# Kernel optimization log

Measured on AMD Instinct MI355X. Metric: run time of the kernel, lower is better.

The kernel has to match this reference:

```python
import jax, jax.numpy as jnp
import numpy as np

B, N, S = 256, 512, 32
D_ENT, D_KEY, D_IN, D_FUNC, D_TYPE, H = 256, 32, 1024, 256, 259, 32


def _init_linear(k, out_d, in_d):
    kw, kb = jax.random.split(k)
    bound = 1.0 / np.sqrt(in_d)
    W = jax.random.uniform(kw, (out_d, in_d), minval=-bound, maxval=bound, dtype=jnp.float32)
    b = jax.random.uniform(kb, (out_d,), minval=-bound, maxval=bound, dtype=jnp.float32)
    return W, b


def setup_inputs() -> dict:
    key = jax.random.key(0)
    ks = jax.random.split(key, 16)
    inp = {
        "embedding": jax.random.normal(ks[0], (B, D_IN), jnp.float32),
        "available_unit_type_mask": (jax.random.uniform(ks[1], (B, D_TYPE)) < 0.5).astype(jnp.float32),
        "available_units_mask": jnp.ones((B, N), jnp.float32),
        "entity_embedding": jax.random.normal(ks[2], (B, N, D_ENT), jnp.float32),
        "selected_units": jax.random.randint(ks[3], (B, S), 0, N, dtype=jnp.int32),
        "end_embedding": jax.random.uniform(ks[4], (1, D_KEY), minval=-1.0, maxval=1.0, dtype=jnp.float32) / np.sqrt(D_KEY),
    }
    inp["W_key"], inp["b_key"] = _init_linear(ks[5], D_KEY, D_ENT)
    inp["W_func"], inp["b_func"] = _init_linear(ks[6], D_FUNC, D_TYPE)
    inp["W_fc1"], inp["b_fc1"] = _init_linear(ks[7], D_FUNC, D_IN)
    inp["W_fc2"], inp["b_fc2"] = _init_linear(ks[8], D_KEY, D_FUNC)
    inp["W_embed"], inp["b_embed"] = _init_linear(ks[9], D_IN, D_KEY)
    inp["W_ih"], inp["b_ih"] = _init_linear(ks[10], 4 * H, D_KEY)
    inp["W_hh"], inp["b_hh"] = _init_linear(ks[11], 4 * H, H)
    return inp


def reference(embedding, available_unit_type_mask, available_units_mask, entity_embedding,
              selected_units, end_embedding, W_key, b_key, W_func, b_func, W_fc1, b_fc1,
              W_fc2, b_fc2, W_embed, b_embed, W_ih, b_ih, W_hh, b_hh):
    Bv, Nv, _ = entity_embedding.shape
    Sv = selected_units.shape[1]
    # keys for each entity + end-flag embedding appended -> [B, N+1, key_dim]
    key_t = jnp.einsum('bnd,kd->bnk', entity_embedding, W_key) + b_key
    end = jnp.broadcast_to(end_embedding[None, :, :], (Bv, 1, end_embedding.shape[1]))
    pad_key = jnp.concatenate([key_t, end], axis=1)
    # mask: entities + end flag; teacher-forced selected positions forced to 1
    mask0 = jnp.concatenate([available_units_mask, jnp.ones((Bv, 1), available_units_mask.dtype)], axis=1)
    mask0 = mask0.at[jnp.arange(Bv)[:, None], selected_units].set(1.0)
    func_embed = jax.nn.relu(available_unit_type_mask @ W_func.T + b_func)
    inv_n = 1.0 / jnp.float32(Nv)  # split_entity_num = end_flag_index = num_units
    bidx = jnp.arange(Bv)
    # per-step selected index (dummy 0 on the final end-flag step) and validity
    sel_seq = jnp.concatenate([selected_units.T, jnp.zeros((1, Bv), selected_units.dtype)], axis=0)
    valid_seq = jnp.concatenate([jnp.ones((Sv, Bv), jnp.float32), jnp.zeros((1, Bv), jnp.float32)], axis=0)

    def step(carry, xs):
        emb, h, c, mask = carry
        sel, valid = xs
        # query = fc2(relu(fc1(emb) + func_embed))
        x = jax.nn.relu(emb @ W_fc1.T + b_fc1 + func_embed) @ W_fc2.T + b_fc2
        # one LSTM step
        gates = x @ W_ih.T + b_ih + h @ W_hh.T + b_hh
        i_g, f_g, g_g, o_g = jnp.split(gates, 4, axis=1)
        c = jax.nn.sigmoid(f_g) * c + jax.nn.sigmoid(i_g) * jnp.tanh(g_g)
        h = jax.nn.sigmoid(o_g) * jnp.tanh(c)
        # masked dot-product over keys -> logits [B, N+1]
        q = jnp.einsum('bk,bnk->bn', h, pad_key) - (1.0 - mask) * 1e9
        # mark selected unit unavailable for subsequent steps
        mask = mask.at[bidx, sel].set(jnp.where(valid > 0, 0.0, mask[bidx, sel]))
        # one-hot gather of selected key, averaged, fed back into embedding
        emb_sel = pad_key[bidx, sel] * inv_n
        emb = emb + (emb_sel @ W_embed.T + b_embed) * valid[:, None]
        return (emb, h, c, mask), q

    h0 = jnp.zeros((Bv, W_hh.shape[1]), jnp.float32)
    c0 = jnp.zeros_like(h0)
    (emb, _, _, _), logits = jax.lax.scan(step, (embedding, h0, c0, mask0), (sel_seq, valid_seq))
    logits = jnp.transpose(logits, (1, 0, 2))  # [B, S+1, N+1]
    return logits, emb
```

## Files before the change

kernel.cpp:

```cpp
#include <hip/hip_runtime.h>
#include <math.h>

#define BB_ 256
#define NN_ 512
#define SS_ 32
#define NP1 513
#define SP1 33
#define D_IN 1024
#define D_TYPE 259
#define INV_N (1.0f/512.0f)

typedef short s16x4 __attribute__((ext_vector_type(4)));
typedef short s16x8 __attribute__((ext_vector_type(8)));
typedef float f32x4 __attribute__((ext_vector_type(4)));

#if defined(__has_builtin)
#if __has_builtin(__builtin_amdgcn_rcpf)
#define FRCP(x) __builtin_amdgcn_rcpf(x)
#else
#define FRCP(x) (1.0f / (x))
#endif
#else
#define FRCP(x) (1.0f / (x))
#endif

__device__ __forceinline__ float fsig(float x) { return FRCP(1.0f + __expf(-x)); }
__device__ __forceinline__ float ftanh(float x) { return fmaf(-2.0f, FRCP(1.0f + __expf(2.0f * x)), 1.0f); }
__device__ __forceinline__ short f2bf(float f) {
    unsigned u = __float_as_uint(f);
    unsigned r = (u + 0x7FFFu + ((u >> 16) & 1u)) >> 16;
    return (short)r;
}

__global__ __launch_bounds__(256) void prep_kernel(
    const float* __restrict__ Wemb, const float* __restrict__ bemb,
    const float* __restrict__ Wfc1, const float* __restrict__ emb0,
    const float* __restrict__ bfc1, const float* __restrict__ atm,
    const float* __restrict__ Wf, const float* __restrict__ bf,
    float* __restrict__ WcombT, float* __restrict__ cbv,
    float* __restrict__ act_pre)
{
    __shared__ float col[D_IN];
    __shared__ float a_lds[16 * 260];
    __shared__ float w_lds[16 * 260];
    const int tid = threadIdx.x;

    if (blockIdx.x < 33) {
        const int k = blockIdx.x;
        if (k < 32) {
            for (int p = 0; p < 4; p++) col[p * 256 + tid] = Wemb[(size_t)(p * 256 + tid) * 32 + k];
        } else {
            for (int p = 0; p < 4; p++) col[p * 256 + tid] = bemb[p * 256 + tid];
        }
        __syncthreads();
        const float* wr = Wfc1 + (size_t)tid * D_IN;
        float acc = 0.0f;
        for (int i4 = 0; i4 < 256; i4++) {
            float4 wv = *(const float4*)(wr + i4 * 4);
            acc = fmaf(col[i4*4+0], wv.x, acc);
            acc = fmaf(col[i4*4+1], wv.y, acc);
            acc = fmaf(col[i4*4+2], wv.z, acc);
            acc = fmaf(col[i4*4+3], wv.w, acc);
        }
        if (k < 32) WcombT[tid * 32 + k] = acc;
        else        cbv[tid] = acc;
    } else {
        const int idx = blockIdx.x - 33;
        const int jt = idx & 15, bt = idx >> 4;
        const int bb = tid >> 4, jj = tid & 15;

#pragma unroll 4
        for (int r = 0; r < 16; r++) {
            a_lds[r * 260 + tid] = atm[(size_t)(bt * 16 + r) * D_TYPE + tid];
            w_lds[r * 260 + tid] = Wf[(size_t)(jt * 16 + r) * D_TYPE + tid];
            if (tid < 3) {
                a_lds[r * 260 + 256 + tid] = atm[(size_t)(bt * 16 + r) * D_TYPE + 256 + tid];
                w_lds[r * 260 + 256 + tid] = Wf[(size_t)(jt * 16 + r) * D_TYPE + 256 + tid];
            }
        }
        __syncthreads();
        float accf = 0.0f;
        {
            const float4* ap = (const float4*)&a_lds[bb * 260];
            const float4* wp = (const float4*)&w_lds[jj * 260];
#pragma unroll 8
            for (int i4 = 0; i4 < 64; i4++) {
                float4 a = ap[i4]; float4 wv = wp[i4];
                accf = fmaf(a.x, wv.x, accf); accf = fmaf(a.y, wv.y, accf);
                accf = fmaf(a.z, wv.z, accf); accf = fmaf(a.w, wv.w, accf);
            }
            for (int i = 256; i < 259; i++) accf = fmaf(a_lds[bb * 260 + i], w_lds[jj * 260 + i], accf);
        }
        float acc = 0.0f;
        for (int c = 0; c < 4; c++) {
            __syncthreads();
#pragma unroll
            for (int p = 0; p < 4; p++) {
                int l4 = p * 256 + tid;
                int r = l4 >> 6, k4 = l4 & 63;
                *(float4*)&a_lds[r * 260 + k4 * 4] =
                    *(const float4*)(emb0 + (size_t)(bt * 16 + r) * D_IN + c * 256 + k4 * 4);
                *(float4*)&w_lds[r * 260 + k4 * 4] =
                    *(const float4*)(Wfc1 + (size_t)(jt * 16 + r) * D_IN + c * 256 + k4 * 4);
            }
            __syncthreads();
#pragma unroll 8
            for (int k4 = 0; k4 < 64; k4++) {
                float4 a = *(const float4*)&a_lds[bb * 260 + k4 * 4];
                float4 wv = *(const float4*)&w_lds[jj * 260 + k4 * 4];
                acc = fmaf(a.x, wv.x, acc); acc = fmaf(a.y, wv.y, acc);
                acc = fmaf(a.z, wv.z, acc); acc = fmaf(a.w, wv.w, acc);
            }
        }
        const int b = bt * 16 + bb, j = jt * 16 + jj;
        act_pre[b * 256 + j] = acc + bfc1[j] + fmaxf(accf + bf[j], 0.0f);
    }
}

__global__ __launch_bounds__(256, 1) void mega_kernel(
    const float* __restrict__ ent, const float* __restrict__ Wk,
    const float* __restrict__ bk, const float* __restrict__ endv,
    const float* __restrict__ act_pre0, const int* __restrict__ sel,
    const float* __restrict__ Wfc2, const float* __restrict__ bfc2,
    const float* __restrict__ Wih, const float* __restrict__ bih,
    const float* __restrict__ bhh, const float* __restrict__ Whh,
    const float* __restrict__ WcombT, const float* __restrict__ cbv,
    const float* __restrict__ emb0, const float* __restrict__ Wemb,
    const float* __restrict__ bemb, const float* __restrict__ avail,
    float* __restrict__ logits, float* __restrict__ emb_out)
{
    __shared__ float k_l[NP1 * 33];
    __shared__ float u_l[17028];
    __shared__ float x_l[SP1 * 32];
    __shared__ float h_all[SP1 * 32];
    __shared__ float cumE_l[SP1 * 32];
    __shared__ float m0_l[NP1];
    __shared__ int   tf_l[NP1];
    __shared__ float ssel_l[32];

    short* a_st  = (short*)u_l;
    float* rap_l = u_l;
    float* red_l = u_l + 8580;
    float* xg_l  = u_l;

    const int tid = threadIdx.x;
    const int b = blockIdx.x;
    const int lane = tid & 63, w = tid >> 6;
    const int nl = lane & 15, q = lane >> 4;

    {
        s16x8 bfr[8][2];
#pragma unroll
        for (int s = 0; s < 8; s++)
#pragma unroll
            for (int t = 0; t < 2; t++) {
                const float* src = Wk + (size_t)(t * 16 + nl) * 256 + s * 32 + q * 8;
                float4 v0 = *(const float4*)(src);
                float4 v1 = *(const float4*)(src + 4);
                s16x8 bv;
                bv[0] = f2bf(v0.x); bv[1] = f2bf(v0.y); bv[2] = f2bf(v0.z); bv[3] = f2bf(v0.w);
                bv[4] = f2bf(v1.x); bv[5] = f2bf(v1.y); bv[6] = f2bf(v1.z); bv[7] = f2bf(v1.w);
                bfr[s][t] = bv;
            }
        float bkv[2];
        bkv[0] = bk[nl]; bkv[1] = bk[16 + nl];
        const float* entb = ent + (size_t)b * NN_ * 256;

        for (int chunk = 0; chunk < 4; ++chunk) {
            f32x4 acc[2][2];
#pragma unroll
            for (int mt = 0; mt < 2; mt++)
#pragma unroll
                for (int t = 0; t < 2; t++) acc[mt][t] = (f32x4)0.0f;

            for (int kc = 0; kc < 4; ++kc) {
                __syncthreads();
#pragma unroll
                for (int p = 0; p < 8; p++) {
                    int flat = p * 256 + tid;
                    int row = flat >> 4;
                    int f4 = flat & 15;
                    float4 v = *(const float4*)(entb + (size_t)(chunk * 128 + row) * 256 + kc * 64 + f4 * 4);
                    s16x4 sv;
                    sv[0] = f2bf(v.x); sv[1] = f2bf(v.y); sv[2] = f2bf(v.z); sv[3] = f2bf(v.w);
                    *(s16x4*)&a_st[row * 72 + f4 * 4] = sv;
                }
                __syncthreads();
#pragma unroll
                for (int ks = 0; ks < 2; ks++) {
                    const int sg = kc * 2 + ks;
#pragma unroll
                    for (int mt = 0; mt < 2; mt++) {
                        s16x8 af = *(const s16x8*)&a_st[(w * 32 + mt * 16 + nl) * 72 + ks * 32 + q * 8];
#pragma unroll
                        for (int t = 0; t < 2; t++)
                            acc[mt][t] = __builtin_amdgcn_mfma_f32_16x16x32_bf16(af, bfr[sg][t], acc[mt][t], 0, 0, 0);
                    }
                }
            }
#pragma unroll
            for (int mt = 0; mt < 2; mt++)
#pragma unroll
                for (int t = 0; t < 2; t++)
#pragma unroll
                    for (int r = 0; r < 4; r++) {
                        int n = chunk * 128 + w * 32 + mt * 16 + q * 4 + r;
                        k_l[n * 33 + t * 16 + nl] = acc[mt][t][r] + bkv[t];
                    }
        }
        if (tid < 32) k_l[512 * 33 + tid] = endv[tid];
        for (int n = tid; n < NP1; n += 256) {
            m0_l[n] = (n < NN_) ? avail[(size_t)b * NN_ + n] : 1.0f;
            tf_l[n] = 1000;
        }
    }
    __syncthreads();

    {
        const int k = tid & 31, sq = tid >> 5;
        const int sq4 = sq * 4;
        float v0, v1, v2, v3;
        {
            int s0 = sel[b * SS_ + sq4 + 0];
            int s1 = sel[b * SS_ + sq4 + 1];
            int s2 = sel[b * SS_ + sq4 + 2];
            int s3 = sel[b * SS_ + sq4 + 3];
            v0 = k_l[s0 * 33 + k] * INV_N;
            v1 = k_l[s1 * 33 + k] * INV_N;
            v2 = k_l[s2 * 33 + k] * INV_N;
            v3 = k_l[s3 * 33 + k] * INV_N;
        }
        float p0 = v0, p1 = p0 + v1, p2 = p1 + v2, p3 = p2 + v3;
        x_l[sq * 32 + k] = p3;
        if (tid < SS_) {
            int n = sel[b * SS_ + tid];
            m0_l[n] = 1.0f;
            atomicMin(&tf_l[n], tid);
        }
        __syncthreads();
        float off = 0.0f;
        for (int p = 0; p < 8; p++) if (p < sq) off += x_l[p * 32 + k];
        cumE_l[(sq4 + 1) * 32 + k] = off + p0;
        cumE_l[(sq4 + 2) * 32 + k] = off + p1;
        cumE_l[(sq4 + 3) * 32 + k] = off + p2;
        cumE_l[(sq4 + 4) * 32 + k] = off + p3;
        if (tid < 32) cumE_l[tid] = 0.0f;
        if (sq == 7) ssel_l[k] = off + p3;
    }
    __syncthreads();

    {
        float wcr[32];
#pragma unroll
        for (int k4 = 0; k4 < 8; k4++) {
            float4 v = *(const float4*)(WcombT + (size_t)tid * 32 + k4 * 4);
            wcr[k4*4] = v.x; wcr[k4*4+1] = v.y; wcr[k4*4+2] = v.z; wcr[k4*4+3] = v.w;
        }
        const float cbr = cbv[tid];
        const float ap0v = act_pre0[b * 256 + tid];
        for (int t = 0; t < SP1; ++t) {
            float ap = fmaf((float)t, cbr, ap0v);
            const float4* ce = (const float4*)&cumE_l[t * 32];
#pragma unroll
            for (int k4 = 0; k4 < 8; k4++) {
                float4 e = ce[k4];
                ap = fmaf(e.x, wcr[k4*4], ap);   ap = fmaf(e.y, wcr[k4*4+1], ap);
                ap = fmaf(e.z, wcr[k4*4+2], ap); ap = fmaf(e.w, wcr[k4*4+3], ap);
            }
            rap_l[t * 260 + tid] = fmaxf(ap, 0.0f);
        }
    }
    __syncthreads();

    {
        const int seg = tid >> 5, i = tid & 31;
        float wfc2r[32];
#pragma unroll
        for (int i4 = 0; i4 < 8; i4++) {
            float4 v = *(const float4*)(Wfc2 + (size_t)i * 256 + seg * 32 + i4 * 4);
            wfc2r[i4*4] = v.x; wfc2r[i4*4+1] = v.y; wfc2r[i4*4+2] = v.z; wfc2r[i4*4+3] = v.w;
        }
        for (int t = 0; t < SP1; ++t) {
            float part = 0.0f;
            const float4* rp = (const float4*)&rap_l[t * 260 + seg * 32];
#pragma unroll
            for (int i4 = 0; i4 < 8; i4++) {
                float4 rv = rp[i4];
                part = fmaf(rv.x, wfc2r[i4*4], part);   part = fmaf(rv.y, wfc2r[i4*4+1], part);
                part = fmaf(rv.z, wfc2r[i4*4+2], part); part = fmaf(rv.w, wfc2r[i4*4+3], part);
            }
            red_l[t * 256 + seg * 32 + i] = part;
        }
    }
    __syncthreads();

    for (int p = 0; p < 5; p++) {
        int idx = p * 256 + tid;
        if (idx < SP1 * 32) {
            int t = idx >> 5, i = idx & 31;
            float x = bfc2[i];
#pragma unroll
            for (int s = 0; s < 8; s++) x += red_l[t * 256 + s * 32 + i];
            x_l[t * 32 + i] = x;
        }
    }
    __syncthreads();

    {
        const int g = tid & 127, half = tid >> 7;
        float wihr[32];
#pragma unroll
        for (int k4 = 0; k4 < 8; k4++) {
            float4 v = *(const float4*)(Wih + (size_t)g * 32 + k4 * 4);
            wihr[k4*4] = v.x; wihr[k4*4+1] = v.y; wihr[k4*4+2] = v.z; wihr[k4*4+3] = v.w;
        }
        const float bihg = bih[g] + bhh[g];
        for (int t = half; t < SP1; t += 2) {
            float gg = bihg;
            const float4* xp = (const float4*)&x_l[t * 32];
#pragma unroll
            for (int k4 = 0; k4 < 8; k4++) {
                float4 xv = xp[k4];
                gg = fmaf(xv.x, wihr[k4*4], gg);   gg = fmaf(xv.y, wihr[k4*4+1], gg);
                gg = fmaf(xv.z, wihr[k4*4+2], gg); gg = fmaf(xv.w, wihr[k4*4+3], gg);
            }
            xg_l[t * 128 + g] = gg;
        }
    }
    __syncthreads();

    if (tid < 64) {
        float whh0[32], whh1[32];
#pragma unroll
        for (int k4 = 0; k4 < 8; k4++) {
            float4 v0 = *(const float4*)(Whh + (size_t)tid * 32 + k4 * 4);
            float4 v1 = *(const float4*)(Whh + (size_t)(tid + 64) * 32 + k4 * 4);
            whh0[k4*4] = v0.x; whh0[k4*4+1] = v0.y; whh0[k4*4+2] = v0.z; whh0[k4*4+3] = v0.w;
            whh1[k4*4] = v1.x; whh1[k4*4+1] = v1.y; whh1[k4*4+2] = v1.z; whh1[k4*4+3] = v1.w;
        }
        float c = 0.0f, h = 0.0f;
        for (int t = 0; t < SP1; ++t) {
            float g0 = xg_l[t * 128 + tid];
            float g1 = xg_l[t * 128 + 64 + tid];
            if (t > 0) {
#pragma unroll
                for (int k = 0; k < 32; k++) {
                    float hk = __shfl(h, k);
                    g0 = fmaf(hk, whh0[k], g0);
                    g1 = fmaf(hk, whh1[k], g1);
                }
            }
            float og0 = __shfl_xor(g0, 32);
            float og1 = __shfl_xor(g1, 32);
            float ig = fsig(g0);
            float fg = fsig(og0);
            float gv = ftanh(g1);
            float og = fsig(og1);
            float cn = fg * c + ig * gv;
            float hn = og * ftanh(cn);
            if (tid < 32) {
                c = cn; h = hn;
                h_all[t * 32 + tid] = hn;
            }
        }
    }
    __syncthreads();

    {
        s16x8 afr[3];
#pragma unroll
        for (int mt = 0; mt < 3; mt++) {
            int row = mt * 16 + nl;
            s16x8 av;
#pragma unroll
            for (int jj = 0; jj < 8; jj++) {
                float v = (row < SP1) ? h_all[row * 32 + q * 8 + jj] : 0.0f;
                av[jj] = f2bf(v);
            }
            afr[mt] = av;
        }
        for (int nt = w; nt < 33; nt += 4) {
            int n = nt * 16 + nl;
            s16x8 bv;
#pragma unroll
            for (int jj = 0; jj < 8; jj++) {
                float v = (n < NP1) ? k_l[n * 33 + q * 8 + jj] : 0.0f;
                bv[jj] = f2bf(v);
            }
            f32x4 acc[3];
#pragma unroll
            for (int mt = 0; mt < 3; mt++)
                acc[mt] = __builtin_amdgcn_mfma_f32_16x16x32_bf16(afr[mt], bv, (f32x4)0.0f, 0, 0, 0);
            float m0v = (n < NP1) ? m0_l[n] : 0.0f;
            int tfv = (n < NP1) ? tf_l[n] : 0;
#pragma unroll
            for (int mt = 0; mt < 3; mt++)
#pragma unroll
                for (int r = 0; r < 4; r++) {
                    int t = mt * 16 + q * 4 + r;
                    if (t < SP1 && n < NP1) {
                        float mv = (t <= tfv) ? m0v : 0.0f;
                        logits[((size_t)b * SP1 + t) * NP1 + n] = acc[mt][r] - (1.0f - mv) * 1e9f;
                    }
                }
        }
    }

#pragma unroll
    for (int p = 0; p < 4; p++) {
        int i = p * 256 + tid;
        float acc = emb0[(size_t)b * D_IN + i] + 32.0f * bemb[i];
        const float* wr = Wemb + (size_t)i * 32;
#pragma unroll
        for (int k4 = 0; k4 < 8; k4++) {
            float4 wv = *(const float4*)(wr + k4 * 4);
            acc = fmaf(ssel_l[k4*4+0], wv.x, acc);
            acc = fmaf(ssel_l[k4*4+1], wv.y, acc);
            acc = fmaf(ssel_l[k4*4+2], wv.z, acc);
            acc = fmaf(ssel_l[k4*4+3], wv.w, acc);
        }
        emb_out[(size_t)b * D_IN + i] = acc;
    }
}

extern "C" void kernel_launch(void* const* d_in, const int* in_sizes, int n_in,
                              void* d_out, int out_size, void* d_ws, size_t ws_size,
                              hipStream_t stream)
{
    (void)in_sizes; (void)n_in; (void)out_size; (void)ws_size;
    const float* embedding = (const float*)d_in[0];
    const float* atm       = (const float*)d_in[1];
    const float* avail     = (const float*)d_in[2];
    const float* ent       = (const float*)d_in[3];
    const int*   sel       = (const int*)  d_in[4];
    const float* endv      = (const float*)d_in[5];
    const float* Wk   = (const float*)d_in[6];
    const float* bk   = (const float*)d_in[7];
    const float* Wf   = (const float*)d_in[8];
    const float* bf   = (const float*)d_in[9];
    const float* Wfc1 = (const float*)d_in[10];
    const float* bfc1 = (const float*)d_in[11];
    const float* Wfc2 = (const float*)d_in[12];
    const float* bfc2 = (const float*)d_in[13];
    const float* Wemb = (const float*)d_in[14];
    const float* bemb = (const float*)d_in[15];
    const float* Wih  = (const float*)d_in[16];
    const float* bih  = (const float*)d_in[17];
    const float* Whh  = (const float*)d_in[18];
    const float* bhh  = (const float*)d_in[19];

    float* ws = (float*)d_ws;
    float* act_pre = ws;
    float* WcombT  = act_pre + BB_ * 256;
    float* cbv     = WcombT + 256 * 32;

    float* logits  = (float*)d_out;
    float* emb_out = logits + (size_t)BB_ * SP1 * NP1;

    prep_kernel<<<289, 256, 0, stream>>>(Wemb, bemb, Wfc1, embedding, bfc1,
                                         atm, Wf, bf, WcombT, cbv, act_pre);
    mega_kernel<<<BB_, 256, 0, stream>>>(ent, Wk, bk, endv, act_pre, sel,
                                         Wfc2, bfc2, Wih, bih, bhh, Whh,
                                         WcombT, cbv, embedding, Wemb, bemb,
                                         avail, logits, emb_out);
}
```

Baseline: 318.4 us.

## Split fused mega kernel into key, scan, and logits kernels for parallelism

Breaks the per-batch mega kernel into separate kernels. A 1024-block key projection kernel writes bf16 keys to workspace, a scan kernel runs the LSTM recurrence and writes bf16 hidden states, and a 1024-block logits kernel computes the masked logits. The goal is to spread the large entity projection and the logits store over more blocks than the 256 one-per-batch blocks, and to shrink LDS use in the serial scan kernel. In exchange it adds global round-trips for keys and hidden states plus extra launch overhead. Teacher-forced mask indices are now found by a per-entity linear search instead of atomics.

```diff
diff --git a/kernel.cpp b/kernel.cpp
--- a/kernel.cpp
+++ b/kernel.cpp
@@ -31,19 +31,105 @@
     unsigned r = (u + 0x7FFFu + ((u >> 16) & 1u)) >> 16;
     return (short)r;
 }
+__device__ __forceinline__ float bf2f(short s) {
+    unsigned u = ((unsigned)(unsigned short)s) << 16;
+    return __uint_as_float(u);
+}
+
+__global__ __launch_bounds__(256) void key_kernel(
+    const float* __restrict__ ent, const float* __restrict__ Wk,
+    const float* __restrict__ bk, short* __restrict__ pkbf)
+{
+    __shared__ short a_lds[128 * 72];
+    const int tid = threadIdx.x;
+    const int lane = tid & 63, w = tid >> 6;
+    const int nl = lane & 15, q = lane >> 4;
+    const size_t rowbase = (size_t)blockIdx.x * 128;
+
+    s16x8 bfr[8][2];
+#pragma unroll
+    for (int s = 0; s < 8; s++)
+#pragma unroll
+        for (int t = 0; t < 2; t++) {
+            const float* src = Wk + (size_t)(t * 16 + nl) * 256 + s * 32 + q * 8;
+            float4 v0 = *(const float4*)(src);
+            float4 v1 = *(const float4*)(src + 4);
+            s16x8 bv;
+            bv[0] = f2bf(v0.x); bv[1] = f2bf(v0.y); bv[2] = f2bf(v0.z); bv[3] = f2bf(v0.w);
+            bv[4] = f2bf(v1.x); bv[5] = f2bf(v1.y); bv[6] = f2bf(v1.z); bv[7] = f2bf(v1.w);
+            bfr[s][t] = bv;
+        }
+
+    f32x4 acc[2][2];
+#pragma unroll
+    for (int mt = 0; mt < 2; mt++)
+#pragma unroll
+        for (int t = 0; t < 2; t++) acc[mt][t] = (f32x4)0.0f;
+
+    for (int kc = 0; kc < 4; ++kc) {
+        __syncthreads();
+#pragma unroll
+        for (int p = 0; p < 8; p++) {
+            int flat = p * 256 + tid;
+            int row = flat >> 4;
+            int f4 = flat & 15;
+            float4 v = *(const float4*)(ent + (rowbase + row) * 256 + kc * 64 + f4 * 4);
+            s16x4 sv;
+            sv[0] = f2bf(v.x); sv[1] = f2bf(v.y); sv[2] = f2bf(v.z); sv[3] = f2bf(v.w);
+            *(s16x4*)&a_lds[row * 72 + f4 * 4] = sv;
+        }
+        __syncthreads();
+#pragma unroll
+        for (int ks = 0; ks < 2; ks++) {
+            const int sg = kc * 2 + ks;
+#pragma unroll
+            for (int mt = 0; mt < 2; mt++) {
+                s16x8 af = *(const s16x8*)&a_lds[(w * 32 + mt * 16 + nl) * 72 + ks * 32 + q * 8];
+#pragma unroll
+                for (int t = 0; t < 2; t++)
+                    acc[mt][t] = __builtin_amdgcn_mfma_f32_16x16x32_bf16(af, bfr[sg][t], acc[mt][t], 0, 0, 0);
+            }
+        }
+    }
+
+    float bkv[2];
+    bkv[0] = bk[nl]; bkv[1] = bk[16 + nl];
+#pragma unroll
+    for (int mt = 0; mt < 2; mt++)
+#pragma unroll
+        for (int t = 0; t < 2; t++)
+#pragma unroll
+            for (int r = 0; r < 4; r++) {
+                int rowg = (int)rowbase + w * 32 + mt * 16 + q * 4 + r;
+                int b = rowg >> 9, n = rowg & 511;
+                pkbf[((size_t)b * NP1 + n) * 32 + t * 16 + nl] = f2bf(acc[mt][t][r] + bkv[t]);
+            }
+}
 
 __global__ __launch_bounds__(256) void prep_kernel(
     const float* __restrict__ Wemb, const float* __restrict__ bemb,
     const float* __restrict__ Wfc1, const float* __restrict__ emb0,
     const float* __restrict__ bfc1, const float* __restrict__ atm,
     const float* __restrict__ Wf, const float* __restrict__ bf,
+    const float* __restrict__ endv,
     float* __restrict__ WcombT, float* __restrict__ cbv,
-    float* __restrict__ act_pre)
+    float* __restrict__ act_pre, short* __restrict__ pkbf)
 {
     __shared__ float col[D_IN];
     __shared__ float a_lds[16 * 260];
     __shared__ float w_lds[16 * 260];
     const int tid = threadIdx.x;
+
+    if (blockIdx.x == 289) {
+        short ev = 0;
+        if (tid < 32) ev = f2bf(endv[tid]);
+        const int k = tid & 31, b0 = tid >> 5;
+        short evk = f2bf(endv[k]);
+        for (int b = b0; b < BB_; b += 8)
+            pkbf[((size_t)b * NP1 + 512) * 32 + k] = evk;
+        (void)ev;
+        return;
+    }
 
     if (blockIdx.x < 33) {
         const int k = blockIdx.x;
@@ -117,126 +203,40 @@
     }
 }
 
-__global__ __launch_bounds__(256, 1) void mega_kernel(
-    const float* __restrict__ ent, const float* __restrict__ Wk,
-    const float* __restrict__ bk, const float* __restrict__ endv,
-    const float* __restrict__ act_pre0, const int* __restrict__ sel,
+__global__ __launch_bounds__(256, 1) void scan_kernel(
+    const short* __restrict__ pkbf, const float* __restrict__ act_pre0,
+    const int* __restrict__ sel,
     const float* __restrict__ Wfc2, const float* __restrict__ bfc2,
     const float* __restrict__ Wih, const float* __restrict__ bih,
     const float* __restrict__ bhh, const float* __restrict__ Whh,
     const float* __restrict__ WcombT, const float* __restrict__ cbv,
     const float* __restrict__ emb0, const float* __restrict__ Wemb,
-    const float* __restrict__ bemb, const float* __restrict__ avail,
-    float* __restrict__ logits, float* __restrict__ emb_out)
+    const float* __restrict__ bemb,
+    short* __restrict__ h_bf, float* __restrict__ emb_out)
 {
-    __shared__ float k_l[NP1 * 33];
-    __shared__ float u_l[17028];
+    __shared__ float rap_l[SP1 * 260];
+    __shared__ float red_l[SP1 * 256];
+    __shared__ float xg_l[SP1 * 128];
     __shared__ float x_l[SP1 * 32];
-    __shared__ float h_all[SP1 * 32];
     __shared__ float cumE_l[SP1 * 32];
-    __shared__ float m0_l[NP1];
-    __shared__ int   tf_l[NP1];
     __shared__ float ssel_l[32];
-
-    short* a_st  = (short*)u_l;
-    float* rap_l = u_l;
-    float* red_l = u_l + 8580;
-    float* xg_l  = u_l;
 
     const int tid = threadIdx.x;
     const int b = blockIdx.x;
-    const int lane = tid & 63, w = tid >> 6;
-    const int nl = lane & 15, q = lane >> 4;
-
-    {
-        s16x8 bfr[8][2];
-#pragma unroll
-        for (int s = 0; s < 8; s++)
-#pragma unroll
-            for (int t = 0; t < 2; t++) {
-                const float* src = Wk + (size_t)(t * 16 + nl) * 256 + s * 32 + q * 8;
-                float4 v0 = *(const float4*)(src);
-                float4 v1 = *(const float4*)(src + 4);
-                s16x8 bv;
-                bv[0] = f2bf(v0.x); bv[1] = f2bf(v0.y); bv[2] = f2bf(v0.z); bv[3] = f2bf(v0.w);
-                bv[4] = f2bf(v1.x); bv[5] = f2bf(v1.y); bv[6] = f2bf(v1.z); bv[7] = f2bf(v1.w);
-                bfr[s][t] = bv;
-            }
-        float bkv[2];
-        bkv[0] = bk[nl]; bkv[1] = bk[16 + nl];
-        const float* entb = ent + (size_t)b * NN_ * 256;
-
-        for (int chunk = 0; chunk < 4; ++chunk) {
-            f32x4 acc[2][2];
-#pragma unroll
-            for (int mt = 0; mt < 2; mt++)
-#pragma unroll
-                for (int t = 0; t < 2; t++) acc[mt][t] = (f32x4)0.0f;
-
-            for (int kc = 0; kc < 4; ++kc) {
-                __syncthreads();
-#pragma unroll
-                for (int p = 0; p < 8; p++) {
-                    int flat = p * 256 + tid;
-                    int row = flat >> 4;
-                    int f4 = flat & 15;
-                    float4 v = *(const float4*)(entb + (size_t)(chunk * 128 + row) * 256 + kc * 64 + f4 * 4);
-                    s16x4 sv;
-                    sv[0] = f2bf(v.x); sv[1] = f2bf(v.y); sv[2] = f2bf(v.z); sv[3] = f2bf(v.w);
-                    *(s16x4*)&a_st[row * 72 + f4 * 4] = sv;
-                }
-                __syncthreads();
-#pragma unroll
-                for (int ks = 0; ks < 2; ks++) {
-                    const int sg = kc * 2 + ks;
-#pragma unroll
-                    for (int mt = 0; mt < 2; mt++) {
-                        s16x8 af = *(const s16x8*)&a_st[(w * 32 + mt * 16 + nl) * 72 + ks * 32 + q * 8];
-#pragma unroll
-                        for (int t = 0; t < 2; t++)
-                            acc[mt][t] = __builtin_amdgcn_mfma_f32_16x16x32_bf16(af, bfr[sg][t], acc[mt][t], 0, 0, 0);
-                    }
-                }
-            }
-#pragma unroll
-            for (int mt = 0; mt < 2; mt++)
-#pragma unroll
-                for (int t = 0; t < 2; t++)
-#pragma unroll
-                    for (int r = 0; r < 4; r++) {
-                        int n = chunk * 128 + w * 32 + mt * 16 + q * 4 + r;
-                        k_l[n * 33 + t * 16 + nl] = acc[mt][t][r] + bkv[t];
-                    }
-        }
-        if (tid < 32) k_l[512 * 33 + tid] = endv[tid];
-        for (int n = tid; n < NP1; n += 256) {
-            m0_l[n] = (n < NN_) ? avail[(size_t)b * NN_ + n] : 1.0f;
-            tf_l[n] = 1000;
-        }
-    }
-    __syncthreads();
 
     {
         const int k = tid & 31, sq = tid >> 5;
         const int sq4 = sq * 4;
-        float v0, v1, v2, v3;
-        {
-            int s0 = sel[b * SS_ + sq4 + 0];
-            int s1 = sel[b * SS_ + sq4 + 1];
-            int s2 = sel[b * SS_ + sq4 + 2];
-            int s3 = sel[b * SS_ + sq4 + 3];
-            v0 = k_l[s0 * 33 + k] * INV_N;
-            v1 = k_l[s1 * 33 + k] * INV_N;
-            v2 = k_l[s2 * 33 + k] * INV_N;
-            v3 = k_l[s3 * 33 + k] * INV_N;
-        }
+        int s0 = sel[b * SS_ + sq4 + 0];
+        int s1 = sel[b * SS_ + sq4 + 1];
+        int s2 = sel[b * SS_ + sq4 + 2];
+        int s3 = sel[b * SS_ + sq4 + 3];
+        float v0 = bf2f(pkbf[((size_t)b * NP1 + s0) * 32 + k]) * INV_N;
+        float v1 = bf2f(pkbf[((size_t)b * NP1 + s1) * 32 + k]) * INV_N;
+        float v2 = bf2f(pkbf[((size_t)b * NP1 + s2) * 32 + k]) * INV_N;
+        float v3 = bf2f(pkbf[((size_t)b * NP1 + s3) * 32 + k]) * INV_N;
         float p0 = v0, p1 = p0 + v1, p2 = p1 + v2, p3 = p2 + v3;
         x_l[sq * 32 + k] = p3;
-        if (tid < SS_) {
-            int n = sel[b * SS_ + tid];
-            m0_l[n] = 1.0f;
-            atomicMin(&tf_l[n], tid);
-        }
         __syncthreads();
         float off = 0.0f;
         for (int p = 0; p < 8; p++) if (p < sq) off += x_l[p * 32 + k];
@@ -360,51 +360,11 @@
             float hn = og * ftanh(cn);
             if (tid < 32) {
                 c = cn; h = hn;
-                h_all[t * 32 + tid] = hn;
-            }
-        }
-    }
-    __syncthreads();
-
-    {
-        s16x8 afr[3];
-#pragma unroll
-        for (int mt = 0; mt < 3; mt++) {
-            int row = mt * 16 + nl;
-            s16x8 av;
-#pragma unroll
-            for (int jj = 0; jj < 8; jj++) {
-                float v = (row < SP1) ? h_all[row * 32 + q * 8 + jj] : 0.0f;
-                av[jj] = f2bf(v);
-            }
-            afr[mt] = av;
-        }
-        for (int nt = w; nt < 33; nt += 4) {
-            int n = nt * 16 + nl;
-            s16x8 bv;
-#pragma unroll
-            for (int jj = 0; jj < 8; jj++) {
-                float v = (n < NP1) ? k_l[n * 33 + q * 8 + jj] : 0.0f;
-                bv[jj] = f2bf(v);
-            }
-            f32x4 acc[3];
-#pragma unroll
-            for (int mt = 0; mt < 3; mt++)
-                acc[mt] = __builtin_amdgcn_mfma_f32_16x16x32_bf16(afr[mt], bv, (f32x4)0.0f, 0, 0, 0);
-            float m0v = (n < NP1) ? m0_l[n] : 0.0f;
-            int tfv = (n < NP1) ? tf_l[n] : 0;
-#pragma unroll
-            for (int mt = 0; mt < 3; mt++)
-#pragma unroll
-                for (int r = 0; r < 4; r++) {
-                    int t = mt * 16 + q * 4 + r;
-                    if (t < SP1 && n < NP1) {
-                        float mv = (t <= tfv) ? m0v : 0.0f;
-                        logits[((size_t)b * SP1 + t) * NP1 + n] = acc[mt][r] - (1.0f - mv) * 1e9f;
-                    }
-                }
-        }
-    }
+                h_bf[((size_t)b * SP1 + t) * 32 + tid] = f2bf(hn);
+            }
+        }
+    }
+    __syncthreads();
 
 #pragma unroll
     for (int p = 0; p < 4; p++) {
@@ -420,6 +380,71 @@
             acc = fmaf(ssel_l[k4*4+3], wv.w, acc);
         }
         emb_out[(size_t)b * D_IN + i] = acc;
+    }
+}
+
+__global__ __launch_bounds__(256) void logits_kernel(
+    const short* __restrict__ pkbf, const short* __restrict__ h_bf,
+    const float* __restrict__ avail, const int* __restrict__ sel,
+    float* __restrict__ logits)
+{
+    __shared__ float m0_l[144];
+    __shared__ int   tf_l[144];
+    __shared__ int   sel_l[SS_];
+    const int tid = threadIdx.x;
+    const int b = blockIdx.x, chunk = blockIdx.y;
+    const int base_n = chunk * 128;
+    const int cnt = (chunk == 3) ? 129 : 128;
+    const int lane = tid & 63, w = tid >> 6;
+    const int nl = lane & 15, q = lane >> 4;
+
+    if (tid < SS_) sel_l[tid] = sel[b * SS_ + tid];
+    if (tid < cnt) {
+        int n = base_n + tid;
+        m0_l[tid] = (n < NN_) ? avail[(size_t)b * NN_ + n] : 1.0f;
+        tf_l[tid] = 1000;
+    }
+    __syncthreads();
+    if (tid < cnt) {
+        int n = base_n + tid;
+        int tf = 1000; bool hit = false;
+#pragma unroll 8
+        for (int s = 0; s < SS_; s++) {
+            if (sel_l[s] == n) { hit = true; if (s < tf) tf = s; }
+        }
+        if (hit) { m0_l[tid] = 1.0f; tf_l[tid] = tf; }
+    }
+    __syncthreads();
+
+    s16x8 afr[3];
+#pragma unroll
+    for (int mt = 0; mt < 3; mt++) {
+        int row = mt * 16 + nl;
+        if (row < SP1) afr[mt] = *(const s16x8*)(h_bf + ((size_t)b * SP1 + row) * 32 + q * 8);
+        else           afr[mt] = (s16x8)0;
+    }
+
+    const int ntiles = (cnt + 15) >> 4;
+    for (int tt = w; tt < ntiles; tt += 4) {
+        int n = base_n + tt * 16 + nl;
+        bool nv = (tt * 16 + nl) < cnt;
+        s16x8 bv = nv ? *(const s16x8*)(pkbf + ((size_t)b * NP1 + n) * 32 + q * 8) : (s16x8)0;
+        f32x4 acc[3];
+#pragma unroll
+        for (int mt = 0; mt < 3; mt++)
+            acc[mt] = __builtin_amdgcn_mfma_f32_16x16x32_bf16(afr[mt], bv, (f32x4)0.0f, 0, 0, 0);
+        float m0v = nv ? m0_l[tt * 16 + nl] : 0.0f;
+        int tfv = nv ? tf_l[tt * 16 + nl] : 0;
+#pragma unroll
+        for (int mt = 0; mt < 3; mt++)
+#pragma unroll
+            for (int r = 0; r < 4; r++) {
+                int t = mt * 16 + q * 4 + r;
+                if (t < SP1 && nv) {
+                    float mv = (t <= tfv) ? m0v : 0.0f;
+                    logits[((size_t)b * SP1 + t) * NP1 + n] = acc[mt][r] - (1.0f - mv) * 1e9f;
+                }
+            }
     }
 }
 
@@ -453,14 +478,17 @@
     float* act_pre = ws;
     float* WcombT  = act_pre + BB_ * 256;
     float* cbv     = WcombT + 256 * 32;
+    short* pkbf    = (short*)(cbv + 256);
+    short* h_bf    = pkbf + (size_t)BB_ * NP1 * 32;
 
     float* logits  = (float*)d_out;
     float* emb_out = logits + (size_t)BB_ * SP1 * NP1;
 
-    prep_kernel<<<289, 256, 0, stream>>>(Wemb, bemb, Wfc1, embedding, bfc1,
-                                         atm, Wf, bf, WcombT, cbv, act_pre);
-    mega_kernel<<<BB_, 256, 0, stream>>>(ent, Wk, bk, endv, act_pre, sel,
-                                         Wfc2, bfc2, Wih, bih, bhh, Whh,
-                                         WcombT, cbv, embedding, Wemb, bemb,
-                                         avail, logits, emb_out);
-}
+    key_kernel<<<1024, 256, 0, stream>>>(ent, Wk, bk, pkbf);
+    prep_kernel<<<290, 256, 0, stream>>>(Wemb, bemb, Wfc1, embedding, bfc1,
+                                         atm, Wf, bf, endv, WcombT, cbv, act_pre, pkbf);
+    scan_kernel<<<BB_, 256, 0, stream>>>(pkbf, act_pre, sel, Wfc2, bfc2,
+                                         Wih, bih, bhh, Whh, WcombT, cbv,
+                                         embedding, Wemb, bemb, h_bf, emb_out);
+    logits_kernel<<<dim3(BB_, 4), 256, 0, stream>>>(pkbf, h_bf, avail, sel, logits);
+}
```

New measurement: 323.3 us. No clear change (+1.5%).

## Move entity key projection to wide front kernel and pass bf16 keys

Applied to the files above, without the earlier changes.

The entity key projection (ent @ Wk^T) moves out of the per-batch serial mega kernel into a front kernel spread over 1024 blocks. Each block handles 128 rows and writes bf16 keys to a workspace, which the back kernel reads directly for the gather and the logits MFMA. The Wfc1·Wemb combination is now done with MFMA in two blocks instead of 33 scalar blocks, and the mask/teacher-forcing setup runs on idle waves during the LSTM. This spreads the memory-bound projection over the whole GPU and shrinks LDS use in the back kernel, at the cost of an extra global round trip for keys. The keys are stored at bf16 precision, but the old code already converted them to bf16 before the logits MFMA.

```diff
diff --git a/kernel.cpp b/kernel.cpp
--- a/kernel.cpp
+++ b/kernel.cpp
@@ -31,41 +31,162 @@
     unsigned r = (u + 0x7FFFu + ((u >> 16) & 1u)) >> 16;
     return (short)r;
 }
-
-__global__ __launch_bounds__(256) void prep_kernel(
+__device__ __forceinline__ float bf2f(short s) {
+    unsigned u = ((unsigned)(unsigned short)s) << 16;
+    return __uint_as_float(u);
+}
+
+__global__ __launch_bounds__(256) void front_kernel(
+    const float* __restrict__ ent, const float* __restrict__ Wk,
+    const float* __restrict__ bk, const float* __restrict__ endv,
     const float* __restrict__ Wemb, const float* __restrict__ bemb,
     const float* __restrict__ Wfc1, const float* __restrict__ emb0,
     const float* __restrict__ bfc1, const float* __restrict__ atm,
     const float* __restrict__ Wf, const float* __restrict__ bf,
-    float* __restrict__ WcombT, float* __restrict__ cbv,
-    float* __restrict__ act_pre)
+    short* __restrict__ pkbf, float* __restrict__ WcombT,
+    float* __restrict__ cbv, float* __restrict__ act_pre)
 {
-    __shared__ float col[D_IN];
-    __shared__ float a_lds[16 * 260];
-    __shared__ float w_lds[16 * 260];
+    __shared__ char u_raw[33280];
+    short* a_st   = (short*)u_raw;
+    float* wemb_s = (float*)(u_raw + 18688);
+    float* a_lds  = (float*)u_raw;
+    float* w_lds  = (float*)(u_raw + 16640);
+
     const int tid = threadIdx.x;
-
-    if (blockIdx.x < 33) {
-        const int k = blockIdx.x;
-        if (k < 32) {
-            for (int p = 0; p < 4; p++) col[p * 256 + tid] = Wemb[(size_t)(p * 256 + tid) * 32 + k];
-        } else {
-            for (int p = 0; p < 4; p++) col[p * 256 + tid] = bemb[p * 256 + tid];
-        }
-        __syncthreads();
-        const float* wr = Wfc1 + (size_t)tid * D_IN;
-        float acc = 0.0f;
-        for (int i4 = 0; i4 < 256; i4++) {
-            float4 wv = *(const float4*)(wr + i4 * 4);
-            acc = fmaf(col[i4*4+0], wv.x, acc);
-            acc = fmaf(col[i4*4+1], wv.y, acc);
-            acc = fmaf(col[i4*4+2], wv.z, acc);
-            acc = fmaf(col[i4*4+3], wv.w, acc);
-        }
-        if (k < 32) WcombT[tid * 32 + k] = acc;
-        else        cbv[tid] = acc;
+    const int bid = blockIdx.x;
+    const int lane = tid & 63, w = tid >> 6;
+    const int nl = lane & 15, q = lane >> 4;
+
+    if (bid < 1024) {
+        const size_t rowbase = (size_t)bid * 128;
+        s16x8 bfr[8][2];
+#pragma unroll
+        for (int s = 0; s < 8; s++)
+#pragma unroll
+            for (int t = 0; t < 2; t++) {
+                const float* src = Wk + (size_t)(t * 16 + nl) * 256 + s * 32 + q * 8;
+                float4 v0 = *(const float4*)(src);
+                float4 v1 = *(const float4*)(src + 4);
+                s16x8 bv;
+                bv[0] = f2bf(v0.x); bv[1] = f2bf(v0.y); bv[2] = f2bf(v0.z); bv[3] = f2bf(v0.w);
+                bv[4] = f2bf(v1.x); bv[5] = f2bf(v1.y); bv[6] = f2bf(v1.z); bv[7] = f2bf(v1.w);
+                bfr[s][t] = bv;
+            }
+        f32x4 acc[2][2];
+#pragma unroll
+        for (int mt = 0; mt < 2; mt++)
+#pragma unroll
+            for (int t = 0; t < 2; t++) acc[mt][t] = (f32x4)0.0f;
+
+        for (int kc = 0; kc < 4; ++kc) {
+            __syncthreads();
+#pragma unroll
+            for (int p = 0; p < 8; p++) {
+                int flat = p * 256 + tid;
+                int row = flat >> 4;
+                int f4 = flat & 15;
+                float4 v = *(const float4*)(ent + (rowbase + row) * 256 + kc * 64 + f4 * 4);
+                s16x4 sv;
+                sv[0] = f2bf(v.x); sv[1] = f2bf(v.y); sv[2] = f2bf(v.z); sv[3] = f2bf(v.w);
+                *(s16x4*)&a_st[row * 72 + f4 * 4] = sv;
+            }
+            __syncthreads();
+#pragma unroll
+            for (int ks = 0; ks < 2; ks++) {
+                const int sg = kc * 2 + ks;
+#pragma unroll
+                for (int mt = 0; mt < 2; mt++) {
+                    s16x8 af = *(const s16x8*)&a_st[(w * 32 + mt * 16 + nl) * 72 + ks * 32 + q * 8];
+#pragma unroll
+                    for (int t = 0; t < 2; t++)
+                        acc[mt][t] = __builtin_amdgcn_mfma_f32_16x16x32_bf16(af, bfr[sg][t], acc[mt][t], 0, 0, 0);
+                }
+            }
+        }
+        float bkv[2];
+        bkv[0] = bk[nl]; bkv[1] = bk[16 + nl];
+#pragma unroll
+        for (int mt = 0; mt < 2; mt++)
+#pragma unroll
+            for (int t = 0; t < 2; t++)
+#pragma unroll
+                for (int r = 0; r < 4; r++) {
+                    int rowg = (int)rowbase + w * 32 + mt * 16 + q * 4 + r;
+                    int b = rowg >> 9, n = rowg & 511;
+                    pkbf[((size_t)b * NP1 + n) * 32 + t * 16 + nl] = f2bf(acc[mt][t][r] + bkv[t]);
+                }
+    } else if (bid < 1026) {
+        const int m0 = bid - 1024;
+        f32x4 acc[2][3];
+#pragma unroll
+        for (int mt = 0; mt < 2; mt++)
+#pragma unroll
+            for (int t = 0; t < 3; t++) acc[mt][t] = (f32x4)0.0f;
+
+        for (int kc = 0; kc < 16; ++kc) {
+            __syncthreads();
+#pragma unroll
+            for (int p = 0; p < 8; p++) {
+                int flat = p * 256 + tid;
+                int row = flat >> 4;
+                int f4 = flat & 15;
+                float4 v = *(const float4*)(Wfc1 + (size_t)(m0 * 128 + row) * D_IN + kc * 64 + f4 * 4);
+                s16x4 sv;
+                sv[0] = f2bf(v.x); sv[1] = f2bf(v.y); sv[2] = f2bf(v.z); sv[3] = f2bf(v.w);
+                *(s16x4*)&a_st[row * 72 + f4 * 4] = sv;
+            }
+            {
+                int r = tid >> 2, c0 = tid & 3;
+#pragma unroll
+                for (int cc = 0; cc < 9; cc++) {
+                    int col = c0 + cc * 4;
+                    if (col < 33) {
+                        float v = (col < 32) ? Wemb[(size_t)(kc * 64 + r) * 32 + col]
+                                             : bemb[kc * 64 + r];
+                        wemb_s[r * 33 + col] = v;
+                    }
+                }
+            }
+            __syncthreads();
+#pragma unroll
+            for (int ks = 0; ks < 2; ks++) {
+                s16x8 bv[3];
+#pragma unroll
+                for (int t = 0; t < 3; t++) {
+                    int n = t * 16 + nl;
+#pragma unroll
+                    for (int jj = 0; jj < 8; jj++) {
+                        float v = (n < 33) ? wemb_s[(ks * 32 + q * 8 + jj) * 33 + n] : 0.0f;
+                        bv[t][jj] = f2bf(v);
+                    }
+                }
+#pragma unroll
+                for (int mt = 0; mt < 2; mt++) {
+                    s16x8 af = *(const s16x8*)&a_st[(w * 32 + mt * 16 + nl) * 72 + ks * 32 + q * 8];
+#pragma unroll
+                    for (int t = 0; t < 3; t++)
+                        acc[mt][t] = __builtin_amdgcn_mfma_f32_16x16x32_bf16(af, bv[t], acc[mt][t], 0, 0, 0);
+                }
+            }
+        }
+#pragma unroll
+        for (int mt = 0; mt < 2; mt++)
+#pragma unroll
+            for (int t = 0; t < 3; t++)
+#pragma unroll
+                for (int r = 0; r < 4; r++) {
+                    int j = m0 * 128 + w * 32 + mt * 16 + q * 4 + r;
+                    int n = t * 16 + nl;
+                    if (n < 32) WcombT[j * 32 + n] = acc[mt][t][r];
+                    else if (n == 32) cbv[j] = acc[mt][t][r];
+                }
+    } else if (bid == 1026) {
+        const int k = tid & 31, b0 = tid >> 5;
+        short evk = f2bf(endv[k]);
+        for (int b = b0; b < BB_; b += 8)
+            pkbf[((size_t)b * NP1 + 512) * 32 + k] = evk;
     } else {
-        const int idx = blockIdx.x - 33;
+        const int idx = bid - 1027;
         const int jt = idx & 15, bt = idx >> 4;
         const int bb = tid >> 4, jj = tid & 15;
 
@@ -117,126 +238,49 @@
     }
 }
 
-__global__ __launch_bounds__(256, 1) void mega_kernel(
-    const float* __restrict__ ent, const float* __restrict__ Wk,
-    const float* __restrict__ bk, const float* __restrict__ endv,
-    const float* __restrict__ act_pre0, const int* __restrict__ sel,
+__global__ __launch_bounds__(256, 1) void back_kernel(
+    const short* __restrict__ pkbf, const float* __restrict__ act_pre0,
+    const int* __restrict__ sel, const float* __restrict__ avail,
     const float* __restrict__ Wfc2, const float* __restrict__ bfc2,
     const float* __restrict__ Wih, const float* __restrict__ bih,
     const float* __restrict__ bhh, const float* __restrict__ Whh,
     const float* __restrict__ WcombT, const float* __restrict__ cbv,
     const float* __restrict__ emb0, const float* __restrict__ Wemb,
-    const float* __restrict__ bemb, const float* __restrict__ avail,
+    const float* __restrict__ bemb,
     float* __restrict__ logits, float* __restrict__ emb_out)
 {
-    __shared__ float k_l[NP1 * 33];
-    __shared__ float u_l[17028];
-    __shared__ float x_l[SP1 * 32];
-    __shared__ float h_all[SP1 * 32];
-    __shared__ float cumE_l[SP1 * 32];
-    __shared__ float m0_l[NP1];
-    __shared__ int   tf_l[NP1];
-    __shared__ float ssel_l[32];
-
-    short* a_st  = (short*)u_l;
-    float* rap_l = u_l;
-    float* red_l = u_l + 8580;
-    float* xg_l  = u_l;
+    __shared__ float S[19204];
+    __shared__ int sel_l[SS_];
+    float* rap_l  = S;
+    float* red_l  = S + 8580;
+    float* x_l    = S + 17028;
+    float* cumE_l = S + 18084;
+    float* ssel_l = S + 19140;
+    float* xg_l   = S;
+    float* h_all  = S + 4224;
+    float* m0_l   = S + 8580;
+    int*   tf_l   = (int*)(S + 9093);
 
     const int tid = threadIdx.x;
     const int b = blockIdx.x;
     const int lane = tid & 63, w = tid >> 6;
     const int nl = lane & 15, q = lane >> 4;
 
-    {
-        s16x8 bfr[8][2];
-#pragma unroll
-        for (int s = 0; s < 8; s++)
-#pragma unroll
-            for (int t = 0; t < 2; t++) {
-                const float* src = Wk + (size_t)(t * 16 + nl) * 256 + s * 32 + q * 8;
-                float4 v0 = *(const float4*)(src);
-                float4 v1 = *(const float4*)(src + 4);
-                s16x8 bv;
-                bv[0] = f2bf(v0.x); bv[1] = f2bf(v0.y); bv[2] = f2bf(v0.z); bv[3] = f2bf(v0.w);
-                bv[4] = f2bf(v1.x); bv[5] = f2bf(v1.y); bv[6] = f2bf(v1.z); bv[7] = f2bf(v1.w);
-                bfr[s][t] = bv;
-            }
-        float bkv[2];
-        bkv[0] = bk[nl]; bkv[1] = bk[16 + nl];
-        const float* entb = ent + (size_t)b * NN_ * 256;
-
-        for (int chunk = 0; chunk < 4; ++chunk) {
-            f32x4 acc[2][2];
-#pragma unroll
-            for (int mt = 0; mt < 2; mt++)
-#pragma unroll
-                for (int t = 0; t < 2; t++) acc[mt][t] = (f32x4)0.0f;
-
-            for (int kc = 0; kc < 4; ++kc) {
-                __syncthreads();
-#pragma unroll
-                for (int p = 0; p < 8; p++) {
-                    int flat = p * 256 + tid;
-                    int row = flat >> 4;
-                    int f4 = flat & 15;
-                    float4 v = *(const float4*)(entb + (size_t)(chunk * 128 + row) * 256 + kc * 64 + f4 * 4);
-                    s16x4 sv;
-                    sv[0] = f2bf(v.x); sv[1] = f2bf(v.y); sv[2] = f2bf(v.z); sv[3] = f2bf(v.w);
-                    *(s16x4*)&a_st[row * 72 + f4 * 4] = sv;
-                }
-                __syncthreads();
-#pragma unroll
-                for (int ks = 0; ks < 2; ks++) {
-                    const int sg = kc * 2 + ks;
-#pragma unroll
-                    for (int mt = 0; mt < 2; mt++) {
-                        s16x8 af = *(const s16x8*)&a_st[(w * 32 + mt * 16 + nl) * 72 + ks * 32 + q * 8];
-#pragma unroll
-                        for (int t = 0; t < 2; t++)
-                            acc[mt][t] = __builtin_amdgcn_mfma_f32_16x16x32_bf16(af, bfr[sg][t], acc[mt][t], 0, 0, 0);
-                    }
-                }
-            }
-#pragma unroll
-            for (int mt = 0; mt < 2; mt++)
-#pragma unroll
-                for (int t = 0; t < 2; t++)
-#pragma unroll
-                    for (int r = 0; r < 4; r++) {
-                        int n = chunk * 128 + w * 32 + mt * 16 + q * 4 + r;
-                        k_l[n * 33 + t * 16 + nl] = acc[mt][t][r] + bkv[t];
-                    }
-        }
-        if (tid < 32) k_l[512 * 33 + tid] = endv[tid];
-        for (int n = tid; n < NP1; n += 256) {
-            m0_l[n] = (n < NN_) ? avail[(size_t)b * NN_ + n] : 1.0f;
-            tf_l[n] = 1000;
-        }
-    }
-    __syncthreads();
+    if (tid < SS_) sel_l[tid] = sel[b * SS_ + tid];
 
     {
         const int k = tid & 31, sq = tid >> 5;
         const int sq4 = sq * 4;
-        float v0, v1, v2, v3;
-        {
-            int s0 = sel[b * SS_ + sq4 + 0];
-            int s1 = sel[b * SS_ + sq4 + 1];
-            int s2 = sel[b * SS_ + sq4 + 2];
-            int s3 = sel[b * SS_ + sq4 + 3];
-            v0 = k_l[s0 * 33 + k] * INV_N;
-            v1 = k_l[s1 * 33 + k] * INV_N;
-            v2 = k_l[s2 * 33 + k] * INV_N;
-            v3 = k_l[s3 * 33 + k] * INV_N;
-        }
+        int s0 = sel[b * SS_ + sq4 + 0];
+        int s1 = sel[b * SS_ + sq4 + 1];
+        int s2 = sel[b * SS_ + sq4 + 2];
+        int s3 = sel[b * SS_ + sq4 + 3];
+        float v0 = bf2f(pkbf[((size_t)b * NP1 + s0) * 32 + k]) * INV_N;
+        float v1 = bf2f(pkbf[((size_t)b * NP1 + s1) * 32 + k]) * INV_N;
+        float v2 = bf2f(pkbf[((size_t)b * NP1 + s2) * 32 + k]) * INV_N;
+        float v3 = bf2f(pkbf[((size_t)b * NP1 + s3) * 32 + k]) * INV_N;
         float p0 = v0, p1 = p0 + v1, p2 = p1 + v2, p3 = p2 + v3;
         x_l[sq * 32 + k] = p3;
-        if (tid < SS_) {
-            int n = sel[b * SS_ + tid];
-            m0_l[n] = 1.0f;
-            atomicMin(&tf_l[n], tid);
-        }
         __syncthreads();
         float off = 0.0f;
         for (int p = 0; p < 8; p++) if (p < sq) off += x_l[p * 32 + k];
@@ -363,6 +407,17 @@
                 h_all[t * 32 + tid] = hn;
             }
         }
+    } else {
+        for (int n = tid - 64; n < NP1; n += 192) {
+            float m = (n < NN_) ? avail[(size_t)b * NN_ + n] : 1.0f;
+            int tf = 1000;
+#pragma unroll 8
+            for (int s = 0; s < SS_; s++) {
+                int sv = sel_l[s];
+                if (sv == n) { m = 1.0f; if (s < tf) tf = s; }
+            }
+            m0_l[n] = m; tf_l[n] = tf;
+        }
     }
     __syncthreads();
 
@@ -379,26 +434,22 @@
             }
             afr[mt] = av;
         }
-        for (int nt = w; nt < 33; nt += 4) {
-            int n = nt * 16 + nl;
-            s16x8 bv;
-#pragma unroll
-            for (int jj = 0; jj < 8; jj++) {
-                float v = (n < NP1) ? k_l[n * 33 + q * 8 + jj] : 0.0f;
-                bv[jj] = f2bf(v);
-            }
+        for (int tt = w; tt < 33; tt += 4) {
+            int n = tt * 16 + nl;
+            bool nv = n < NP1;
+            s16x8 bv = nv ? *(const s16x8*)(pkbf + ((size_t)b * NP1 + n) * 32 + q * 8) : (s16x8)0;
             f32x4 acc[3];
 #pragma unroll
             for (int mt = 0; mt < 3; mt++)
                 acc[mt] = __builtin_amdgcn_mfma_f32_16x16x32_bf16(afr[mt], bv, (f32x4)0.0f, 0, 0, 0);
-            float m0v = (n < NP1) ? m0_l[n] : 0.0f;
-            int tfv = (n < NP1) ? tf_l[n] : 0;
+            float m0v = nv ? m0_l[n] : 0.0f;
+            int tfv = nv ? tf_l[n] : 0;
 #pragma unroll
             for (int mt = 0; mt < 3; mt++)
 #pragma unroll
                 for (int r = 0; r < 4; r++) {
                     int t = mt * 16 + q * 4 + r;
-                    if (t < SP1 && n < NP1) {
+                    if (t < SP1 && nv) {
                         float mv = (t <= tfv) ? m0v : 0.0f;
                         logits[((size_t)b * SP1 + t) * NP1 + n] = acc[mt][r] - (1.0f - mv) * 1e9f;
                     }
@@ -453,14 +504,16 @@
     float* act_pre = ws;
     float* WcombT  = act_pre + BB_ * 256;
     float* cbv     = WcombT + 256 * 32;
+    short* pkbf    = (short*)(cbv + 256);
 
     float* logits  = (float*)d_out;
     float* emb_out = logits + (size_t)BB_ * SP1 * NP1;
 
-    prep_kernel<<<289, 256, 0, stream>>>(Wemb, bemb, Wfc1, embedding, bfc1,
-                                         atm, Wf, bf, WcombT, cbv, act_pre);
-    mega_kernel<<<BB_, 256, 0, stream>>>(ent, Wk, bk, endv, act_pre, sel,
+    front_kernel<<<1283, 256, 0, stream>>>(ent, Wk, bk, endv, Wemb, bemb,
+                                           Wfc1, embedding, bfc1, atm, Wf, bf,
+                                           pkbf, WcombT, cbv, act_pre);
+    back_kernel<<<BB_, 256, 0, stream>>>(pkbf, act_pre, sel, avail,
                                          Wfc2, bfc2, Wih, bih, bhh, Whh,
                                          WcombT, cbv, embedding, Wemb, bemb,
-                                         avail, logits, emb_out);
+                                         logits, emb_out);
 }
```

Result: no change. 312.3 us (-1.9%).
